# Kernel optimization log

Measured on AMD Instinct MI355X. Metric: run time of the kernel, lower is better.

Reference implementation:

```python
import jax, jax.numpy as jnp
import numpy as np
import math

NUM_HEADS = 16


def setup_inputs() -> dict:
    key = jax.random.key(0)
    ks = jax.random.split(key, 5)
    L, B, E = 2048, 2, 1024
    scale = 1.0 / math.sqrt(E)
    return {
        "query": jax.random.normal(ks[0], (L, B, E), jnp.float32),
        "key": jax.random.normal(ks[1], (L, B, E), jnp.float32),
        "value": jax.random.normal(ks[2], (L, B, E), jnp.float32),
        "in_proj_weight": jax.random.normal(ks[3], (3 * E, E), jnp.float32) * scale,
        "in_proj_bias": jnp.zeros((3 * E,), jnp.float32),
        "out_w": jax.random.normal(ks[4], (E, E), jnp.float32) * scale,
        "out_b": jnp.zeros((E,), jnp.float32),
    }


def reference(query, key, value, in_proj_weight, in_proj_bias, out_w, out_b):
    L, Bz, E = query.shape
    S = key.shape[0]
    H = NUM_HEADS
    hd = E // H
    # in-projection: chunk packed weight into q/k/v parts (same math as torch chunk)
    w_q, w_k, w_v = jnp.split(in_proj_weight, 3, axis=0)
    b_q, b_k, b_v = jnp.split(in_proj_bias, 3, axis=0)
    q = query @ w_q.T + b_q            # (L, B, E)
    k = key @ w_k.T + b_k              # (S, B, E)
    v = value @ w_v.T + b_v            # (S, B, E)
    # (L, B*H, hd) -> (B*H, L, hd)
    q = q.reshape(L, Bz * H, hd).transpose(1, 0, 2) / math.sqrt(hd)
    k = k.reshape(S, Bz * H, hd).transpose(1, 0, 2)
    v = v.reshape(S, Bz * H, hd).transpose(1, 0, 2)
    # sigmoid attention (non-softmax), full (B*H, L, S) matrix as in original
    attn = jax.nn.sigmoid(jnp.einsum("bld,bsd->bls", q, k))
    denom = attn.sum(axis=-1, keepdims=True) + 1e-4
    out = jnp.einsum("bls,bsd->bld", attn / denom, v)  # (B*H, L, hd)
    out = out.transpose(1, 0, 2).reshape(L, Bz, E)
    out = out @ out_w.T + out_b
    avg_weights = attn.reshape(Bz, H, L, S).sum(axis=1) / H
    return out, avg_weights
```

## Files before the change

### kernel.cpp

```cpp
#include <hip/hip_runtime.h>
#include <stdint.h>


#define L_SEQ 2048
#define NBATCH 2
#define EMB 1024
#define NHEAD 16
#define HD 64
#define MROWS 4096

typedef __bf16 bf16x8 __attribute__((ext_vector_type(8)));
typedef float f32x4 __attribute__((ext_vector_type(4)));

__device__ __forceinline__ unsigned short f2bf(float f) {
  union { float f; uint32_t u; } v; v.f = f;
  uint32_t u = v.u;
  u += 0x7fffu + ((u >> 16) & 1u);
  return (unsigned short)(u >> 16);
}

__device__ __forceinline__ unsigned short f2bf_fast(float f) {
  union { float f; uint32_t u; } v; v.f = f;
  return (unsigned short)((v.u + 0x8000u) >> 16);
}

__device__ __forceinline__ void gl_lds16(const void* gptr, void* ldsptr) {
  const uint32_t* g = reinterpret_cast<const uint32_t*>(gptr);
  auto* l = reinterpret_cast<__attribute__((address_space(3))) uint32_t*>(
      reinterpret_cast<uintptr_t>(ldsptr));
  __builtin_amdgcn_global_load_lds(g, l, 16, 0, 0);
}

__device__ __forceinline__ f32x4 mfma16(bf16x8 a, bf16x8 b, f32x4 c) {
  return __builtin_amdgcn_mfma_f32_16x16x32_bf16(a, b, c, 0, 0, 0);
}

__device__ __forceinline__ float fast_sigmoid(float x) {
  float e = __expf(-x);
  return __builtin_amdgcn_rcpf(1.0f + e);
}

__global__ __launch_bounds__(256) void k_convert(
    const float* __restrict__ qin, const float* __restrict__ kin,
    const float* __restrict__ vin, const float* __restrict__ win,
    const float* __restrict__ wo,
    unsigned short* __restrict__ Xq, unsigned short* __restrict__ Xk,
    unsigned short* __restrict__ Xv, unsigned short* __restrict__ Wb,
    unsigned short* __restrict__ Wob) {
  const int row = blockIdx.x;
  const int t = threadIdx.x;
  const float* src;
  unsigned short* dst;
  int srow;
  size_t drow;
  if (row < 3 * MROWS) {
    const int which = row >> 12;
    const int m = row & (MROWS - 1);
    const int b = m >> 11, l = m & (L_SEQ - 1);
    srow = l * NBATCH + b;
    drow = (size_t)m;
    src = which == 0 ? qin : (which == 1 ? kin : vin);
    dst = which == 0 ? Xq : (which == 1 ? Xk : Xv);
  } else if (row < 3 * MROWS + 3072) {
    srow = row - 3 * MROWS; drow = (size_t)srow; src = win; dst = Wb;
  } else {
    srow = row - (3 * MROWS + 3072); drow = (size_t)srow; src = wo; dst = Wob;
  }
  const float4 vv = *(const float4*)(src + (size_t)srow * EMB + t * 4);
  ushort4 o;
  o.x = f2bf(vv.x); o.y = f2bf(vv.y); o.z = f2bf(vv.z); o.w = f2bf(vv.w);
  *(ushort4*)(dst + drow * EMB + t * 4) = o;
}

__device__ __forceinline__ void gemm_core(
    const unsigned short* __restrict__ A, const unsigned short* __restrict__ Bm,
    int m0, int n0, unsigned short* sA, unsigned short* sB, f32x4 acc[4][4]) {
  const int tid = threadIdx.x;
  const int wave = tid >> 6;
  const int lane = tid & 63;
  const int quad = lane >> 4;
  const int l16 = lane & 15;
  const int wm = (wave >> 1) * 64;
  const int wn = (wave & 1) * 64;
  const int srow = lane >> 2;
  const int scol = lane & 3;

  for (int mi = 0; mi < 4; ++mi)
    for (int ni = 0; ni < 4; ++ni)
      acc[mi][ni] = (f32x4){0.f, 0.f, 0.f, 0.f};

  for (int k0 = 0; k0 < EMB; k0 += 32) {
    __syncthreads();
    for (int i = 0; i < 2; ++i) {
      const int p = wave * 2 + i;
      const int r = p * 16 + srow;
      const int c = scol ^ ((r >> 1) & 3);
      gl_lds16(A + (size_t)(m0 + r) * EMB + k0 + c * 8, sA + p * 512);
      gl_lds16(Bm + (size_t)(n0 + r) * EMB + k0 + c * 8, sB + p * 512);
    }
    __syncthreads();
    bf16x8 af[4], bfr[4];
    for (int mi = 0; mi < 4; ++mi) {
      const int r = wm + mi * 16 + l16;
      const int cp = quad ^ ((r >> 1) & 3);
      af[mi] = *(const bf16x8*)(sA + r * 32 + cp * 8);
    }
    for (int ni = 0; ni < 4; ++ni) {
      const int r = wn + ni * 16 + l16;
      const int cp = quad ^ ((r >> 1) & 3);
      bfr[ni] = *(const bf16x8*)(sB + r * 32 + cp * 8);
    }
    for (int mi = 0; mi < 4; ++mi)
      for (int ni = 0; ni < 4; ++ni)
        acc[mi][ni] = mfma16(af[mi], bfr[ni], acc[mi][ni]);
  }
}

__global__ __launch_bounds__(256) void k_inproj(
    const unsigned short* __restrict__ Xq, const unsigned short* __restrict__ Xk,
    const unsigned short* __restrict__ Xv, const unsigned short* __restrict__ Wb,
    const float* __restrict__ bias,
    unsigned short* __restrict__ qb, unsigned short* __restrict__ kb,
    unsigned short* __restrict__ vb) {
  __shared__ __attribute__((aligned(16))) unsigned short sA[128 * 32];
  __shared__ __attribute__((aligned(16))) unsigned short sB[128 * 32];
  const int z = blockIdx.z;
  const unsigned short* A = z == 0 ? Xq : (z == 1 ? Xk : Xv);
  const int n0 = blockIdx.x * 128, m0 = blockIdx.y * 128;
  f32x4 acc[4][4];
  gemm_core(A, Wb + (size_t)z * EMB * EMB, m0, n0, sA, sB, acc);

  const int tid = threadIdx.x, wave = tid >> 6, lane = tid & 63;
  const int quad = lane >> 4, l16 = lane & 15;
  const int wm = (wave >> 1) * 64, wn = (wave & 1) * 64;
  const float scale = (z == 0) ? 0.125f : 1.0f;
  unsigned short* dst01 = (z == 0) ? qb : kb;
  for (int ni = 0; ni < 4; ++ni) {
    const int n = n0 + wn + ni * 16 + l16;
    const float bv = bias[z * EMB + n];
    const int h = n >> 6, d = n & 63;
    for (int mi = 0; mi < 4; ++mi) {
      for (int r = 0; r < 4; ++r) {
        const int m = m0 + wm + mi * 16 + quad * 4 + r;
        const int b = m >> 11, l = m & (L_SEQ - 1);
        const unsigned short o = f2bf((acc[mi][ni][r] + bv) * scale);
        if (z == 2)
          vb[((size_t)(b * NHEAD + h) * HD + d) * L_SEQ + l] = o;
        else
          dst01[((size_t)(b * NHEAD + h) * L_SEQ + l) * HD + d] = o;
      }
    }
  }
}

__global__ __launch_bounds__(512) void k_attn(
    const unsigned short* __restrict__ qb, const unsigned short* __restrict__ kb,
    const unsigned short* __restrict__ vb, unsigned short* __restrict__ oh) {
  __shared__ __attribute__((aligned(16))) unsigned short sQ[128 * 64];
  __shared__ __attribute__((aligned(16))) unsigned short sK[64 * 64];
  __shared__ __attribute__((aligned(16))) unsigned short sV[64 * 64];
  __shared__ __attribute__((aligned(16))) unsigned short sP[128 * 72];

  const int bh = blockIdx.x;
  const int b = bh >> 4, h = bh & 15;
  const int l0 = blockIdx.y * 128;
  const unsigned short* qg = qb + ((size_t)bh * L_SEQ + l0) * HD;
  const unsigned short* kg = kb + (size_t)bh * L_SEQ * HD;
  const unsigned short* vg = vb + (size_t)bh * HD * L_SEQ;

  const int tid = threadIdx.x, wave = tid >> 6, lane = tid & 63;
  const int quad = lane >> 4, l16 = lane & 15;
  const int sr8 = lane >> 3, sc8 = lane & 7;
  const int sh = (wave >> 2) * 32;
  const int lq = (wave & 3) * 32;

  for (int i = 0; i < 2; ++i) {
    const int p = wave * 2 + i;
    const int r = p * 8 + sr8;
    const int c = sc8 ^ (r & 7);
    gl_lds16(qg + (size_t)r * HD + c * 8, sQ + p * 512);
  }

  f32x4 oacc[4];
  for (int ni = 0; ni < 4; ++ni) oacc[ni] = (f32x4){0.f, 0.f, 0.f, 0.f};
  f32x4 dacc = (f32x4){0.f, 0.f, 0.f, 0.f};

  bf16x8 ones;
  for (int j = 0; j < 8; ++j) ones[j] = (__bf16)1.0f;

  for (int s0 = 0; s0 < L_SEQ; s0 += 64) {
    __syncthreads();
    if (wave < 4) {
      for (int i = 0; i < 2; ++i) {
        const int p = wave * 2 + i;
        const int r = p * 8 + sr8;
        const int c = sc8 ^ (r & 7);
        gl_lds16(kg + (size_t)(s0 + r) * HD + c * 8, sK + p * 512);
      }
    } else {
      for (int i = 0; i < 2; ++i) {
        const int p = (wave - 4) * 2 + i;
        const int r = p * 8 + sr8;
        const int c = sc8 ^ (r & 7);
        gl_lds16(vg + (size_t)r * L_SEQ + s0 + c * 8, sV + p * 512);
      }
    }
    __syncthreads();

    f32x4 st[2][2];
    for (int smi = 0; smi < 2; ++smi)
      for (int lni = 0; lni < 2; ++lni) st[smi][lni] = (f32x4){0.f, 0.f, 0.f, 0.f};
    for (int kk = 0; kk < HD; kk += 32) {
      bf16x8 a[2], bq[2];
      for (int smi = 0; smi < 2; ++smi) {
        const int r = sh + smi * 16 + l16;
        const int c = ((kk >> 3) + quad) ^ (r & 7);
        a[smi] = *(const bf16x8*)(sK + r * 64 + c * 8);
      }
      for (int lni = 0; lni < 2; ++lni) {
        const int r = lq + lni * 16 + l16;
        const int c = ((kk >> 3) + quad) ^ (r & 7);
        bq[lni] = *(const bf16x8*)(sQ + r * 64 + c * 8);
      }
      for (int smi = 0; smi < 2; ++smi)
        for (int lni = 0; lni < 2; ++lni)
          st[smi][lni] = mfma16(a[smi], bq[lni], st[smi][lni]);
    }

    for (int lni = 0; lni < 2; ++lni) {
      const int lrow = lq + lni * 16 + l16;
      for (int smi = 0; smi < 2; ++smi) {
        uint32_t u[4];
        for (int r = 0; r < 4; ++r) {
          union { float f; uint32_t i; } cv;
          cv.f = fast_sigmoid(st[smi][lni][r]);
          u[r] = cv.i + 0x8000u;
        }
        uint2 pk;
        pk.x = __builtin_amdgcn_perm(u[1], u[0], 0x07060302u);
        pk.y = __builtin_amdgcn_perm(u[3], u[2], 0x07060302u);
        *(uint2*)(sP + (size_t)lrow * 72 + sh + smi * 16 + quad * 4) = pk;
      }
    }
    __syncthreads();

    const int lr = wave * 16 + l16;
    for (int kk = 0; kk < 64; kk += 32) {
      bf16x8 ap = *(const bf16x8*)(sP + (size_t)lr * 72 + kk + quad * 8);
      for (int ni = 0; ni < 4; ++ni) {
        const int rd = ni * 16 + l16;
        const int c = ((kk >> 3) + quad) ^ (rd & 7);
        bf16x8 bv4 = *(const bf16x8*)(sV + rd * 64 + c * 8);
        oacc[ni] = mfma16(ap, bv4, oacc[ni]);
      }
      dacc = mfma16(ap, ones, dacc);
    }
  }

  for (int r = 0; r < 4; ++r) {
    const int lrow = l0 + wave * 16 + quad * 4 + r;
    const float rden = __builtin_amdgcn_rcpf(dacc[r] + 1e-4f);
    unsigned short* dst = oh + ((size_t)(b * L_SEQ + lrow)) * EMB + h * HD;
    for (int ni = 0; ni < 4; ++ni)
      dst[ni * 16 + l16] = f2bf_fast(oacc[ni][r] * rden);
  }
}

__global__ __launch_bounds__(512) void k_avg(
    const unsigned short* __restrict__ qb, const unsigned short* __restrict__ kb,
    float* __restrict__ avg) {
  __shared__ __attribute__((aligned(16))) unsigned short sQ[128 * 64];
  __shared__ __attribute__((aligned(16))) unsigned short sK[128 * 64];
  const int ss0 = blockIdx.x * 128, l0 = blockIdx.y * 128, b = blockIdx.z;
  const int tid = threadIdx.x, wave = tid >> 6, lane = tid & 63;
  const int quad = lane >> 4, l16 = lane & 15;
  const int wm = (wave & 1) * 64, wn = (wave >> 1) * 32;
  const int sr8 = lane >> 3, sc8 = lane & 7;

  f32x4 av[4][2];
  for (int mi = 0; mi < 4; ++mi)
    for (int ni = 0; ni < 2; ++ni) av[mi][ni] = (f32x4){0.f, 0.f, 0.f, 0.f};

  for (int h = 0; h < NHEAD; ++h) {
    const unsigned short* qg = qb + ((size_t)(b * NHEAD + h) * L_SEQ + l0) * HD;
    const unsigned short* kg = kb + ((size_t)(b * NHEAD + h) * L_SEQ + ss0) * HD;
    __syncthreads();
    for (int i = 0; i < 2; ++i) {
      const int p = wave * 2 + i;
      const int r = p * 8 + sr8;
      const int c = sc8 ^ (r & 7);
      gl_lds16(qg + (size_t)r * HD + c * 8, sQ + p * 512);
      gl_lds16(kg + (size_t)r * HD + c * 8, sK + p * 512);
    }
    __syncthreads();
    f32x4 scr[4][2];
    for (int mi = 0; mi < 4; ++mi)
      for (int ni = 0; ni < 2; ++ni) scr[mi][ni] = (f32x4){0.f, 0.f, 0.f, 0.f};
    for (int kk = 0; kk < HD; kk += 32) {
      bf16x8 a[4], bb[2];
      for (int mi = 0; mi < 4; ++mi) {
        const int r = wm + mi * 16 + l16;
        const int c = ((kk >> 3) + quad) ^ (r & 7);
        a[mi] = *(const bf16x8*)(sQ + r * 64 + c * 8);
      }
      for (int ni = 0; ni < 2; ++ni) {
        const int r = wn + ni * 16 + l16;
        const int c = ((kk >> 3) + quad) ^ (r & 7);
        bb[ni] = *(const bf16x8*)(sK + r * 64 + c * 8);
      }
      for (int mi = 0; mi < 4; ++mi)
        for (int ni = 0; ni < 2; ++ni)
          scr[mi][ni] = mfma16(a[mi], bb[ni], scr[mi][ni]);
    }
    for (int mi = 0; mi < 4; ++mi)
      for (int ni = 0; ni < 2; ++ni)
        for (int r = 0; r < 4; ++r)
          av[mi][ni][r] += fast_sigmoid(scr[mi][ni][r]);
  }

  for (int mi = 0; mi < 4; ++mi) {
    for (int r = 0; r < 4; ++r) {
      const int l = l0 + wm + mi * 16 + quad * 4 + r;
      float* dst = avg + ((size_t)b * L_SEQ + l) * L_SEQ + ss0 + wn;
      for (int ni = 0; ni < 2; ++ni)
        dst[ni * 16 + l16] = av[mi][ni][r] * 0.0625f;
    }
  }
}

__global__ __launch_bounds__(256) void k_outproj(
    const unsigned short* __restrict__ OH, const unsigned short* __restrict__ Wob,
    const float* __restrict__ ob, float* __restrict__ out) {
  __shared__ __attribute__((aligned(16))) unsigned short sA[128 * 32];
  __shared__ __attribute__((aligned(16))) unsigned short sB[128 * 32];
  const int n0 = blockIdx.x * 128, m0 = blockIdx.y * 128;
  f32x4 acc[4][4];
  gemm_core(OH, Wob, m0, n0, sA, sB, acc);

  const int tid = threadIdx.x, wave = tid >> 6, lane = tid & 63;
  const int quad = lane >> 4, l16 = lane & 15;
  const int wm = (wave >> 1) * 64, wn = (wave & 1) * 64;
  for (int ni = 0; ni < 4; ++ni) {
    const int n = n0 + wn + ni * 16 + l16;
    const float bv = ob[n];
    for (int mi = 0; mi < 4; ++mi) {
      for (int r = 0; r < 4; ++r) {
        const int m = m0 + wm + mi * 16 + quad * 4 + r;
        const int b = m >> 11, l = m & (L_SEQ - 1);
        out[((size_t)l * NBATCH + b) * EMB + n] = acc[mi][ni][r] + bv;
      }
    }
  }
}

extern "C" void kernel_launch(void* const* d_in, const int* in_sizes, int n_in,
                              void* d_out, int out_size, void* d_ws, size_t ws_size,
                              hipStream_t stream) {
  (void)in_sizes; (void)n_in; (void)out_size;
  const float* qin = (const float*)d_in[0];
  const float* kin = (const float*)d_in[1];
  const float* vin = (const float*)d_in[2];
  const float* w   = (const float*)d_in[3];
  const float* bias = (const float*)d_in[4];
  const float* wo  = (const float*)d_in[5];
  const float* ob  = (const float*)d_in[6];
  float* out = (float*)d_out;

  unsigned short* Xq  = (unsigned short*)d_ws;
  unsigned short* Xk  = Xq + (size_t)MROWS * EMB;
  unsigned short* Xv  = Xk + (size_t)MROWS * EMB;
  unsigned short* Wb  = Xv + (size_t)MROWS * EMB;
  unsigned short* Wob = Wb + (size_t)3 * EMB * EMB;
  unsigned short* qbuf = Wob + (size_t)EMB * EMB;
  unsigned short* kbuf = qbuf + (size_t)MROWS * EMB;
  unsigned short* vbuf = kbuf + (size_t)MROWS * EMB;
  unsigned short* ohb  = vbuf + (size_t)MROWS * EMB;
  const size_t need = ((size_t)MROWS * EMB * 7 + (size_t)4 * EMB * EMB) * 2;
  if (ws_size < need) return;

  k_convert<<<16384, 256, 0, stream>>>(qin, kin, vin, w, wo, Xq, Xk, Xv, Wb, Wob);
  k_inproj<<<dim3(8, 32, 3), 256, 0, stream>>>(Xq, Xk, Xv, Wb, bias, qbuf, kbuf, vbuf);
  k_attn<<<dim3(32, 16), 512, 0, stream>>>(qbuf, kbuf, vbuf, ohb);
  k_avg<<<dim3(16, 16, 2), 512, 0, stream>>>(qbuf, kbuf, out + (size_t)MROWS * EMB);
  k_outproj<<<dim3(8, 32), 256, 0, stream>>>(ohb, Wob, ob, out);
}
```

Baseline: 282.5 us.

## Double-buffer K/V and Q/K LDS tiles with async prefetch in attention kernels

Adds ping-pong LDS buffers to k_attn and k_avg so the next tile (next S-block of K/V, or the next head's Q/K) is issued with global_load_lds before computing on the current one. __syncthreads is replaced with explicit vmcnt waits plus raw s_barrier, so global loads overlap MFMA work. LDS use grows, which may lower occupancy, and the hand-set vmcnt counts must match the exact number of outstanding loads per wave.

```diff
diff --git a/kernel.cpp b/kernel.cpp
--- a/kernel.cpp
+++ b/kernel.cpp
@@ -11,6 +11,15 @@
 
 typedef __bf16 bf16x8 __attribute__((ext_vector_type(8)));
 typedef float f32x4 __attribute__((ext_vector_type(4)));
+
+#define WAITVM(N) asm volatile("s_waitcnt vmcnt(" #N ")" ::: "memory")
+#define WAITLG() asm volatile("s_waitcnt lgkmcnt(0)" ::: "memory")
+#define SBAR()                                  \
+  do {                                          \
+    asm volatile("" ::: "memory");              \
+    __builtin_amdgcn_s_barrier();               \
+    asm volatile("" ::: "memory");              \
+  } while (0)
 
 __device__ __forceinline__ unsigned short f2bf(float f) {
   union { float f; uint32_t u; } v; v.f = f;
@@ -157,8 +166,8 @@
     const unsigned short* __restrict__ qb, const unsigned short* __restrict__ kb,
     const unsigned short* __restrict__ vb, unsigned short* __restrict__ oh) {
   __shared__ __attribute__((aligned(16))) unsigned short sQ[128 * 64];
-  __shared__ __attribute__((aligned(16))) unsigned short sK[64 * 64];
-  __shared__ __attribute__((aligned(16))) unsigned short sV[64 * 64];
+  __shared__ __attribute__((aligned(16))) unsigned short sK[2][64 * 64];
+  __shared__ __attribute__((aligned(16))) unsigned short sV[2][64 * 64];
   __shared__ __attribute__((aligned(16))) unsigned short sP[128 * 72];
 
   const int bh = blockIdx.x;
@@ -180,6 +189,21 @@
     const int c = sc8 ^ (r & 7);
     gl_lds16(qg + (size_t)r * HD + c * 8, sQ + p * 512);
   }
+  if (wave < 4) {
+    for (int i = 0; i < 2; ++i) {
+      const int p = wave * 2 + i;
+      const int r = p * 8 + sr8;
+      const int c = sc8 ^ (r & 7);
+      gl_lds16(kg + (size_t)r * HD + c * 8, sK[0] + p * 512);
+    }
+  } else {
+    for (int i = 0; i < 2; ++i) {
+      const int p = (wave - 4) * 2 + i;
+      const int r = p * 8 + sr8;
+      const int c = sc8 ^ (r & 7);
+      gl_lds16(vg + (size_t)r * L_SEQ + c * 8, sV[0] + p * 512);
+    }
+  }
 
   f32x4 oacc[4];
   for (int ni = 0; ni < 4; ++ni) oacc[ni] = (f32x4){0.f, 0.f, 0.f, 0.f};
@@ -188,24 +212,31 @@
   bf16x8 ones;
   for (int j = 0; j < 8; ++j) ones[j] = (__bf16)1.0f;
 
-  for (int s0 = 0; s0 < L_SEQ; s0 += 64) {
-    __syncthreads();
-    if (wave < 4) {
-      for (int i = 0; i < 2; ++i) {
-        const int p = wave * 2 + i;
-        const int r = p * 8 + sr8;
-        const int c = sc8 ^ (r & 7);
-        gl_lds16(kg + (size_t)(s0 + r) * HD + c * 8, sK + p * 512);
-      }
+  const int NS = L_SEQ / 64;
+  for (int it = 0; it < NS; ++it) {
+    const int cur = it & 1;
+    if (it + 1 < NS) {
+      const int s0n = (it + 1) * 64;
+      if (wave < 4) {
+        for (int i = 0; i < 2; ++i) {
+          const int p = wave * 2 + i;
+          const int r = p * 8 + sr8;
+          const int c = sc8 ^ (r & 7);
+          gl_lds16(kg + (size_t)(s0n + r) * HD + c * 8, sK[cur ^ 1] + p * 512);
+        }
+      } else {
+        for (int i = 0; i < 2; ++i) {
+          const int p = (wave - 4) * 2 + i;
+          const int r = p * 8 + sr8;
+          const int c = sc8 ^ (r & 7);
+          gl_lds16(vg + (size_t)r * L_SEQ + s0n + c * 8, sV[cur ^ 1] + p * 512);
+        }
+      }
+      WAITVM(2);
     } else {
-      for (int i = 0; i < 2; ++i) {
-        const int p = (wave - 4) * 2 + i;
-        const int r = p * 8 + sr8;
-        const int c = sc8 ^ (r & 7);
-        gl_lds16(vg + (size_t)r * L_SEQ + s0 + c * 8, sV + p * 512);
-      }
-    }
-    __syncthreads();
+      WAITVM(0);
+    }
+    SBAR();
 
     f32x4 st[2][2];
     for (int smi = 0; smi < 2; ++smi)
@@ -215,7 +246,7 @@
       for (int smi = 0; smi < 2; ++smi) {
         const int r = sh + smi * 16 + l16;
         const int c = ((kk >> 3) + quad) ^ (r & 7);
-        a[smi] = *(const bf16x8*)(sK + r * 64 + c * 8);
+        a[smi] = *(const bf16x8*)(sK[cur] + r * 64 + c * 8);
       }
       for (int lni = 0; lni < 2; ++lni) {
         const int r = lq + lni * 16 + l16;
@@ -242,7 +273,8 @@
         *(uint2*)(sP + (size_t)lrow * 72 + sh + smi * 16 + quad * 4) = pk;
       }
     }
-    __syncthreads();
+    WAITLG();
+    SBAR();
 
     const int lr = wave * 16 + l16;
     for (int kk = 0; kk < 64; kk += 32) {
@@ -250,11 +282,12 @@
       for (int ni = 0; ni < 4; ++ni) {
         const int rd = ni * 16 + l16;
         const int c = ((kk >> 3) + quad) ^ (rd & 7);
-        bf16x8 bv4 = *(const bf16x8*)(sV + rd * 64 + c * 8);
+        bf16x8 bv4 = *(const bf16x8*)(sV[cur] + rd * 64 + c * 8);
         oacc[ni] = mfma16(ap, bv4, oacc[ni]);
       }
       dacc = mfma16(ap, ones, dacc);
     }
+    SBAR();
   }
 
   for (int r = 0; r < 4; ++r) {
@@ -269,8 +302,8 @@
 __global__ __launch_bounds__(512) void k_avg(
     const unsigned short* __restrict__ qb, const unsigned short* __restrict__ kb,
     float* __restrict__ avg) {
-  __shared__ __attribute__((aligned(16))) unsigned short sQ[128 * 64];
-  __shared__ __attribute__((aligned(16))) unsigned short sK[128 * 64];
+  __shared__ __attribute__((aligned(16))) unsigned short sQ[2][128 * 64];
+  __shared__ __attribute__((aligned(16))) unsigned short sK[2][128 * 64];
   const int ss0 = blockIdx.x * 128, l0 = blockIdx.y * 128, b = blockIdx.z;
   const int tid = threadIdx.x, wave = tid >> 6, lane = tid & 63;
   const int quad = lane >> 4, l16 = lane & 15;
@@ -281,18 +314,38 @@
   for (int mi = 0; mi < 4; ++mi)
     for (int ni = 0; ni < 2; ++ni) av[mi][ni] = (f32x4){0.f, 0.f, 0.f, 0.f};
 
-  for (int h = 0; h < NHEAD; ++h) {
-    const unsigned short* qg = qb + ((size_t)(b * NHEAD + h) * L_SEQ + l0) * HD;
-    const unsigned short* kg = kb + ((size_t)(b * NHEAD + h) * L_SEQ + ss0) * HD;
-    __syncthreads();
+  {
+    const unsigned short* qg = qb + ((size_t)(b * NHEAD) * L_SEQ + l0) * HD;
+    const unsigned short* kg = kb + ((size_t)(b * NHEAD) * L_SEQ + ss0) * HD;
     for (int i = 0; i < 2; ++i) {
       const int p = wave * 2 + i;
       const int r = p * 8 + sr8;
       const int c = sc8 ^ (r & 7);
-      gl_lds16(qg + (size_t)r * HD + c * 8, sQ + p * 512);
-      gl_lds16(kg + (size_t)r * HD + c * 8, sK + p * 512);
-    }
-    __syncthreads();
+      gl_lds16(qg + (size_t)r * HD + c * 8, sQ[0] + p * 512);
+      gl_lds16(kg + (size_t)r * HD + c * 8, sK[0] + p * 512);
+    }
+  }
+
+  for (int h = 0; h < NHEAD; ++h) {
+    const int cur = h & 1;
+    if (h + 1 < NHEAD) {
+      const unsigned short* qg =
+          qb + ((size_t)(b * NHEAD + h + 1) * L_SEQ + l0) * HD;
+      const unsigned short* kg =
+          kb + ((size_t)(b * NHEAD + h + 1) * L_SEQ + ss0) * HD;
+      for (int i = 0; i < 2; ++i) {
+        const int p = wave * 2 + i;
+        const int r = p * 8 + sr8;
+        const int c = sc8 ^ (r & 7);
+        gl_lds16(qg + (size_t)r * HD + c * 8, sQ[cur ^ 1] + p * 512);
+        gl_lds16(kg + (size_t)r * HD + c * 8, sK[cur ^ 1] + p * 512);
+      }
+      WAITVM(4);
+    } else {
+      WAITVM(0);
+    }
+    SBAR();
+
     f32x4 scr[4][2];
     for (int mi = 0; mi < 4; ++mi)
       for (int ni = 0; ni < 2; ++ni) scr[mi][ni] = (f32x4){0.f, 0.f, 0.f, 0.f};
@@ -301,12 +354,12 @@
       for (int mi = 0; mi < 4; ++mi) {
         const int r = wm + mi * 16 + l16;
         const int c = ((kk >> 3) + quad) ^ (r & 7);
-        a[mi] = *(const bf16x8*)(sQ + r * 64 + c * 8);
+        a[mi] = *(const bf16x8*)(sQ[cur] + r * 64 + c * 8);
       }
       for (int ni = 0; ni < 2; ++ni) {
         const int r = wn + ni * 16 + l16;
         const int c = ((kk >> 3) + quad) ^ (r & 7);
-        bb[ni] = *(const bf16x8*)(sK + r * 64 + c * 8);
+        bb[ni] = *(const bf16x8*)(sK[cur] + r * 64 + c * 8);
       }
       for (int mi = 0; mi < 4; ++mi)
         for (int ni = 0; ni < 2; ++ni)
@@ -316,6 +369,7 @@
       for (int ni = 0; ni < 2; ++ni)
         for (int r = 0; r < 4; ++r)
           av[mi][ni][r] += fast_sigmoid(scr[mi][ni][r]);
+    SBAR();
   }
 
   for (int mi = 0; mi < 4; ++mi) {
```

After: 283.5 us. Within noise of the previous version (+0.4%).
